# Kernel optimization log

Hardware: AMD Instinct MI355X
Metric: run time of the kernel (lower is better)

## Reference

```python
import jax, jax.numpy as jnp
import numpy as np
import math

N_BITS = 8
NUM_GROUPS = 32
NUM_HEADS = 8
EPS = 1e-5


def fake_quant(x):
    # UniformAffineQuantizer: dynamic per-tensor asymmetric 8-bit fake quant
    levels = 2 ** N_BITS - 1
    xmin = jnp.minimum(x.min(), 0.0)
    xmax = jnp.maximum(x.max(), 0.0)
    scale = jnp.maximum((xmax - xmin) / levels, 1e-8)
    zp = jnp.round(-xmin / scale)
    xq = jnp.clip(jnp.round(x / scale) + zp, 0, levels)
    return (xq - zp) * scale


def group_norm(x, w, b):
    # x: (B, C, T)
    B, C, T = x.shape
    xg = x.reshape(B, NUM_GROUPS, C // NUM_GROUPS, T)
    mean = xg.mean(axis=(2, 3), keepdims=True)
    var = xg.var(axis=(2, 3), keepdims=True)
    xg = (xg - mean) * jax.lax.rsqrt(var + EPS)
    return xg.reshape(B, C, T) * w[None, :, None] + b[None, :, None]


def setup_inputs() -> dict:
    key = jax.random.key(0)
    ks = jax.random.split(key, 7)
    C = 512
    x = jax.random.normal(ks[0], (8, C, 32, 32), dtype=jnp.float32)
    gn_w = jnp.ones((C,), jnp.float32)
    gn_b = jnp.zeros((C,), jnp.float32)
    qkv_w = jax.random.normal(ks[1], (3 * C, C), jnp.float32) * (1.0 / math.sqrt(C))
    qkv_b = jax.random.normal(ks[2], (3 * C,), jnp.float32) * 0.01
    proj_w = jax.random.normal(ks[3], (C, C), jnp.float32) * (1.0 / math.sqrt(C))
    proj_b = jax.random.normal(ks[4], (C,), jnp.float32) * 0.01
    return {"x": x, "gn_w": gn_w, "gn_b": gn_b, "qkv_w": qkv_w,
            "qkv_b": qkv_b, "proj_w": proj_w, "proj_b": proj_b}


def reference(x, gn_w, gn_b, qkv_w, qkv_b, proj_w, proj_b):
    b, c, *spatial = x.shape
    T = int(np.prod(spatial))
    xf = x.reshape(b, c, T)                       # (B, C, T)
    h = group_norm(xf, gn_w, gn_b)
    qkv = jnp.einsum('oc,bct->bot', qkv_w, h) + qkv_b[None, :, None]  # (B, 3C, T)
    qkv = qkv.reshape(b * NUM_HEADS, -1, T)       # (B*H, 3*ch, T)
    ch = qkv.shape[1] // 3
    q, k, v = jnp.split(qkv, 3, axis=1)
    q = fake_quant(q)
    k = fake_quant(k)
    v = fake_quant(v)
    scale = 1.0 / math.sqrt(math.sqrt(ch))
    w = jnp.einsum('bct,bcs->bts', q * scale, k * scale)
    w = jax.nn.softmax(w.astype(jnp.float32), axis=-1).astype(q.dtype)
    a = jnp.einsum('bts,bcs->bct', w, v)          # (B*H, ch, T)
    a = a.reshape(b, c, T)
    a = jnp.einsum('oc,bct->bot', proj_w, a) + proj_b[None, :, None]
    return (xf + a).reshape(b, c, *spatial)
```

## Files before the change

kernel.cpp:

```cpp
#include <hip/hip_runtime.h>

typedef __attribute__((ext_vector_type(8))) __bf16 bf16x8;
typedef __attribute__((ext_vector_type(4))) __bf16 bf16x4;
typedef __attribute__((ext_vector_type(4))) float  f32x4;


static constexpr size_t QKV_OFF = 0;
static constexpr size_t HT_OFF  = 50331648;
static constexpr size_t WQ_OFF  = HT_OFF + 8388608;
static constexpr size_t WP_OFF  = WQ_OFF + 1572864;
static constexpr size_t MM_OFF  = WP_OFF + 524288;
static constexpr size_t KI_OFF  = MM_OFF + 8192;
static constexpr size_t VI_OFF  = KI_OFF + 8388608;
static constexpr size_t QI_OFF  = VI_OFF + 8388608;
static constexpr size_t NEED_NEW = QI_OFF + 8388608;

__device__ __forceinline__ float dqi(float x, float inv_s, float zp) {
    float y = rintf(x * inv_s);
    return fminf(fmaxf(y, -zp), 255.0f - zp);
}
__device__ __forceinline__ f32x4 mfma16(bf16x8 a, bf16x8 b, f32x4 c) {
    return __builtin_amdgcn_mfma_f32_16x16x32_bf16(a, b, c, 0, 0, 0);
}
__device__ __forceinline__ float exp2i(float x) {
    float r;
    asm("v_exp_f32 %0, %1" : "=v"(r) : "v"(x));
    return r;
}
__device__ __forceinline__ void glds16(const __bf16* g, __bf16* l) {
    __builtin_amdgcn_global_load_lds((const __attribute__((address_space(1))) void*)g,
                                     (__attribute__((address_space(3))) void*)l, 16, 0, 0);
}
template <int N> __device__ __forceinline__ void waitv() {
    asm volatile("s_waitcnt vmcnt(%0)" :: "n"(N) : "memory");
}
__device__ __forceinline__ void bar_raw() {
    asm volatile("s_barrier" ::: "memory");
}

__device__ __forceinline__ void red_mm(const float* __restrict__ pmm, int id, int tid,
                                       float* sred, float& mn_out, float& mx_out) {
    float mn = pmm[id * 512 + tid * 2];
    float mx = pmm[id * 512 + tid * 2 + 1];
#pragma unroll
    for (int m = 1; m < 64; m <<= 1) {
        mn = fminf(mn, __shfl_xor(mn, m));
        mx = fmaxf(mx, __shfl_xor(mx, m));
    }
    if ((tid & 63) == 0) { sred[(tid >> 6) * 2] = mn; sred[(tid >> 6) * 2 + 1] = mx; }
    __syncthreads();
    mn = fminf(fminf(sred[0], sred[2]), fminf(sred[4], sred[6]));
    mx = fmaxf(fmaxf(sred[1], sred[3]), fmaxf(sred[5], sred[7]));
    __syncthreads();
    mn_out = fminf(mn, 0.0f);
    mx_out = fmaxf(mx, 0.0f);
}

__global__ __launch_bounds__(256) void gnprep(const float* __restrict__ x,
                                              const float* __restrict__ w,
                                              const float* __restrict__ bv,
                                              __bf16* __restrict__ hT,
                                              const float* __restrict__ qw,
                                              __bf16* __restrict__ wq,
                                              const float* __restrict__ pw,
                                              __bf16* __restrict__ wp) {
    int bid = blockIdx.x, tid = threadIdx.x;
    if (bid < 1024) {
        if (bid < 768) {
            int i = bid * 256 + tid;
            float4 v = ((const float4*)qw)[i];
            bf16x4 o = {(__bf16)v.x, (__bf16)v.y, (__bf16)v.z, (__bf16)v.w};
            ((bf16x4*)wq)[i] = o;
        } else {
            int i = (bid - 768) * 256 + tid;
            float4 v = ((const float4*)pw)[i];
            bf16x4 o = {(__bf16)v.x, (__bf16)v.y, (__bf16)v.z, (__bf16)v.w};
            ((bf16x4*)wp)[i] = o;
        }
        return;
    }
    int blk = bid - 1024;
    int b = blk >> 5, g = blk & 31;
    const float* xp = x + (size_t)(b * 512 + g * 16) * 1024;

    float4 v[16];
    float sum = 0.f, ss = 0.f;
#pragma unroll
    for (int i = 0; i < 16; ++i) {
        v[i] = *(const float4*)(xp + (size_t)i * 1024 + tid * 4);
        sum += v[i].x + v[i].y + v[i].z + v[i].w;
        ss  += v[i].x * v[i].x + v[i].y * v[i].y + v[i].z * v[i].z + v[i].w * v[i].w;
    }
#pragma unroll
    for (int m = 1; m < 64; m <<= 1) {
        sum += __shfl_xor(sum, m);
        ss  += __shfl_xor(ss, m);
    }
    __shared__ float s1[4], s2[4];
    int wid = tid >> 6;
    if ((tid & 63) == 0) { s1[wid] = sum; s2[wid] = ss; }
    __syncthreads();
    sum = s1[0] + s1[1] + s1[2] + s1[3];
    ss  = s2[0] + s2[1] + s2[2] + s2[3];
    float mean = sum * (1.0f / 16384.0f);
    float var  = ss * (1.0f / 16384.0f) - mean * mean;
    float rstd = rsqrtf(var + 1e-5f);

    float wc[16], bc[16];
#pragma unroll
    for (int c = 0; c < 16; ++c) { wc[c] = w[g * 16 + c] * rstd; bc[c] = bv[g * 16 + c]; }

#pragma unroll
    for (int j = 0; j < 4; ++j) {
        int t = tid * 4 + j;
        bf16x8 o0, o1;
#pragma unroll
        for (int c = 0; c < 8; ++c)
            o0[c] = (__bf16)(((&v[c].x)[j] - mean) * wc[c] + bc[c]);
#pragma unroll
        for (int c = 0; c < 8; ++c)
            o1[c] = (__bf16)(((&v[c + 8].x)[j] - mean) * wc[c + 8] + bc[c + 8]);
        __bf16* hp = hT + ((size_t)b * 1024 + t) * 512 + g * 16;
        *(bf16x8*)hp = o0;
        *(bf16x8*)(hp + 8) = o1;
    }
}

template <int MTILE, int MOT, bool MINMAX, bool RESID>
__global__ __launch_bounds__(256, 2) void mgemm5(const __bf16* __restrict__ A,
                                                 const __bf16* __restrict__ Bt,
                                                 const float* __restrict__ bias,
                                                 const float* __restrict__ resid,
                                                 float* __restrict__ out,
                                                 int M, float* __restrict__ pmm) {
    constexpr int NF  = (MTILE == 128) ? 4 : 2;
    constexpr int ASZ = MTILE * 64;
    constexpr int BSZ = 128 * 64;
    constexpr int LA  = MTILE / 32;
    constexpr int L   = LA + 4;
    constexpr int STG = 2 * (ASZ + BSZ) * 2;
    constexpr int CSB = 64 * 132 * 4;
    __shared__ __attribute__((aligned(16))) char smem_raw[(STG > CSB) ? STG : CSB];
    __bf16* sA0 = (__bf16*)smem_raw;
    __bf16* sA1 = sA0 + ASZ;
    __bf16* sB0 = sA1 + ASZ;
    __bf16* sB1 = sB0 + BSZ;
    __shared__ float smn[4], smx[4];

    int tid = threadIdx.x;
    int l = tid & 63, w = tid >> 6;
    int lo = l & 15, hi = l >> 4;

    int f = blockIdx.x;
    constexpr int NWG = MOT * 64;
    int wg = (f & 7) * (NWG / 8) + (f >> 3);
    int mo = wg % MOT, nb = wg / MOT;
    int nt = nb & 7, b = nb >> 3;

    const __bf16* Ap = A + (size_t)mo * MTILE * 512;
    const __bf16* Bp = Bt + ((size_t)b * 1024 + (size_t)nt * 128) * 512;
    int m0 = (MTILE == 128) ? (w >> 1) * 64 : 0;
    int n0 = (MTILE == 128) ? (w & 1) * 64 : w * 32;
    f32x4 acc[4][NF] = {};
    int scd = tid & 7;

    auto STAGE = [&](__bf16* dA, __bf16* dB, int k0) {
#pragma unroll
        for (int p = 0; p < LA; ++p) {
            int lin = p * 2048 + tid * 8;
            int row = lin >> 6;
            glds16(Ap + (size_t)row * 512 + k0 + ((scd ^ (row & 7)) << 3), dA + lin);
        }
#pragma unroll
        for (int p = 0; p < 4; ++p) {
            int lin = p * 2048 + tid * 8;
            int row = lin >> 6;
            glds16(Bp + (size_t)row * 512 + k0 + ((scd ^ (row & 7)) << 3), dB + lin);
        }
    };
    auto COMPUTE = [&](const __bf16* cA, const __bf16* cB) {
#pragma unroll
        for (int kk = 0; kk < 2; ++kk) {
            int rch = ((kk * 4 + hi) ^ (lo & 7)) << 3;
            bf16x8 af[4], bfr[NF];
#pragma unroll
            for (int i = 0; i < 4; ++i) af[i] = *(const bf16x8*)&cA[(m0 + 16 * i + lo) * 64 + rch];
#pragma unroll
            for (int j = 0; j < NF; ++j) bfr[j] = *(const bf16x8*)&cB[(n0 + 16 * j + lo) * 64 + rch];
#pragma unroll
            for (int i = 0; i < 4; ++i)
#pragma unroll
                for (int j = 0; j < NF; ++j) acc[i][j] = mfma16(af[i], bfr[j], acc[i][j]);
        }
    };

    STAGE(sA0, sB0, 0);
#pragma unroll
    for (int kp = 0; kp < 8; kp += 2) {
        if (kp + 1 < 8) { STAGE(sA1, sB1, (kp + 1) * 64); waitv<L>(); } else { waitv<0>(); }
        bar_raw();
        COMPUTE(sA0, sB0);
        bar_raw();
        if (kp + 2 < 8) { STAGE(sA0, sB0, (kp + 2) * 64); waitv<L>(); } else { waitv<0>(); }
        bar_raw();
        COMPUTE(sA1, sB1);
        bar_raw();
    }

    float* cs = (float*)smem_raw;
    float mn = 1e30f, mx = -1e30f;
    constexpr int NH = (MTILE == 128) ? 2 : 1;
#pragma unroll
    for (int h = 0; h < NH; ++h) {
        __syncthreads();
        if (MTILE == 64 || (w >> 1) == h) {
#pragma unroll
            for (int i = 0; i < 4; ++i)
#pragma unroll
                for (int r = 0; r < 4; ++r) {
                    int rl = 16 * i + hi * 4 + r;
                    float bi = bias[mo * MTILE + h * 64 + rl];
#pragma unroll
                    for (int j = 0; j < NF; ++j)
                        cs[rl * 132 + n0 + 16 * j + lo] = acc[i][j][r] + bi;
                }
        }
        __syncthreads();
#pragma unroll
        for (int it = 0; it < 8; ++it) {
            int lin = it * 256 + tid;
            int rr = lin >> 5, cc = (lin & 31) << 2;
            float4 v = *(const float4*)&cs[rr * 132 + cc];
            if (MINMAX) {
                mn = fminf(mn, fminf(fminf(v.x, v.y), fminf(v.z, v.w)));
                mx = fmaxf(mx, fmaxf(fmaxf(v.x, v.y), fmaxf(v.z, v.w)));
            }
            int grow = mo * MTILE + h * 64 + rr;
            size_t gaddr = ((size_t)b * M + grow) * 1024 + nt * 128 + cc;
            if (RESID) {
                float4 rv = *(const float4*)&resid[gaddr];
                v.x += rv.x; v.y += rv.y; v.z += rv.z; v.w += rv.w;
            }
            *(float4*)&out[gaddr] = v;
        }
    }

    if (MINMAX) {
#pragma unroll
        for (int msk = 1; msk < 64; msk <<= 1) {
            mn = fminf(mn, __shfl_xor(mn, msk));
            mx = fmaxf(mx, __shfl_xor(mx, msk));
        }
        if (l == 0) { smn[w] = mn; smx[w] = mx; }
        __syncthreads();
        if (tid == 0) {
            mn = fminf(fminf(smn[0], smn[1]), fminf(smn[2], smn[3]));
            mx = fmaxf(fmaxf(smx[0], smx[1]), fmaxf(smx[2], smx[3]));
            int id = mo >> 2;
            int slot = nb * 4 + (mo & 3);
            pmm[id * 512 + slot * 2]     = mn;
            pmm[id * 512 + slot * 2 + 1] = mx;
        }
    }
}

__global__ __launch_bounds__(256) void quant_qkv(const float* __restrict__ qkv,
                                                 const float* __restrict__ pmm,
                                                 __bf16* __restrict__ qi,
                                                 __bf16* __restrict__ ki,
                                                 __bf16* __restrict__ vi) {
    int bh = blockIdx.x, tt = blockIdx.y;
    int b = bh >> 3, hh = bh & 7;
    int t0 = tt * 64;
    const float* qg = qkv + (size_t)(b * 1536 + hh * 192) * 1024;
    const float* kg = qg + 65536;
    const float* vg = qg + 131072;
    int tid = threadIdx.x;

    __shared__ float sred[8];
    float mn0, mx0, mn1, mx1, mn2, mx2;
    red_mm(pmm, 0, tid, sred, mn0, mx0);
    red_mm(pmm, 1, tid, sred, mn1, mx1);
    red_mm(pmm, 2, tid, sred, mn2, mx2);
    float qsc = fmaxf((mx0 - mn0) * (1.f / 255.f), 1e-8f), qzp = rintf(-mn0 / qsc);
    float ksc = fmaxf((mx1 - mn1) * (1.f / 255.f), 1e-8f), kzp = rintf(-mn1 / ksc);
    float vsc = fmaxf((mx2 - mn2) * (1.f / 255.f), 1e-8f), vzp = rintf(-mn2 / vsc);
    float inv_q = 1.f / qsc, inv_k = 1.f / ksc, inv_v = 1.f / vsc;

    __shared__ __bf16 sT[64][68];
    int cr = tid >> 4, t4 = tid & 15;
    int s = tid >> 2, c0 = (tid & 3) * 16;

    __bf16* vd = vi + (size_t)bh * 65536;
#pragma unroll
    for (int r = 0; r < 4; ++r) {
        int c = 16 * r + cr;
        float4 v = *(const float4*)(vg + (size_t)c * 1024 + t0 + t4 * 4);
        bf16x4 o = {(__bf16)dqi(v.x, inv_v, vzp), (__bf16)dqi(v.y, inv_v, vzp),
                    (__bf16)dqi(v.z, inv_v, vzp), (__bf16)dqi(v.w, inv_v, vzp)};
        *(bf16x4*)(vd + (size_t)c * 1024 + t0 + t4 * 4) = o;
    }

#pragma unroll
    for (int r = 0; r < 4; ++r) {
        int c = 16 * r + cr;
        float4 v = *(const float4*)(kg + (size_t)c * 1024 + t0 + t4 * 4);
        sT[t4 * 4 + 0][c] = (__bf16)dqi(v.x, inv_k, kzp);
        sT[t4 * 4 + 1][c] = (__bf16)dqi(v.y, inv_k, kzp);
        sT[t4 * 4 + 2][c] = (__bf16)dqi(v.z, inv_k, kzp);
        sT[t4 * 4 + 3][c] = (__bf16)dqi(v.w, inv_k, kzp);
    }
    __syncthreads();
    {
        bf16x8 a0 = *(const bf16x8*)&sT[s][c0];
        bf16x8 a1 = *(const bf16x8*)&sT[s][c0 + 8];
        __bf16* kd = ki + ((size_t)bh * 1024 + t0 + s) * 64 + c0;
        *(bf16x8*)kd = a0;
        *(bf16x8*)(kd + 8) = a1;
    }
    __syncthreads();

#pragma unroll
    for (int r = 0; r < 4; ++r) {
        int c = 16 * r + cr;
        float4 v = *(const float4*)(qg + (size_t)c * 1024 + t0 + t4 * 4);
        sT[t4 * 4 + 0][c] = (__bf16)dqi(v.x, inv_q, qzp);
        sT[t4 * 4 + 1][c] = (__bf16)dqi(v.y, inv_q, qzp);
        sT[t4 * 4 + 2][c] = (__bf16)dqi(v.z, inv_q, qzp);
        sT[t4 * 4 + 3][c] = (__bf16)dqi(v.w, inv_q, qzp);
    }
    __syncthreads();
    {
        bf16x8 a0 = *(const bf16x8*)&sT[s][c0];
        bf16x8 a1 = *(const bf16x8*)&sT[s][c0 + 8];
        __bf16* qd = qi + ((size_t)bh * 1024 + t0 + s) * 64 + c0;
        *(bf16x8*)qd = a0;
        *(bf16x8*)(qd + 8) = a1;
    }
}

__global__ __launch_bounds__(256) void attn4(const __bf16* __restrict__ qi,
                                             const __bf16* __restrict__ ki,
                                             const __bf16* __restrict__ vi,
                                             const float* __restrict__ pmm,
                                             __bf16* __restrict__ aT) {
    int f = blockIdx.x;
    int bh = (f & 7) * 8 + ((f >> 3) & 7);
    int tt = f >> 6;
    int b = bh >> 3, hh = bh & 7;
    int t0 = tt * 64;
    const __bf16* kb = ki + (size_t)bh * 65536;
    const __bf16* vb = vi + (size_t)bh * 65536;
    int tid = threadIdx.x;

    __shared__ float sred[8];
    float mn0, mx0, mn1, mx1, mn2, mx2;
    red_mm(pmm, 0, tid, sred, mn0, mx0);
    red_mm(pmm, 1, tid, sred, mn1, mx1);
    red_mm(pmm, 2, tid, sred, mn2, mx2);
    float qsc = fmaxf((mx0 - mn0) * (1.f / 255.f), 1e-8f);
    float ksc = fmaxf((mx1 - mn1) * (1.f / 255.f), 1e-8f);
    float vsc = fmaxf((mx2 - mn2) * (1.f / 255.f), 1e-8f);
    float alpha2 = qsc * ksc * 0.125f * 1.4426950408889634f;
    float thr = 11.5415603f / alpha2;

    __shared__ __bf16 sh[64][72];
    __shared__ __bf16 kS[64 * 64];
    __shared__ __bf16 vS[64 * 64];
    int l = tid & 63, w = tid >> 6;
    int lo = l & 15, hi = l >> 4;

    const __bf16* qrow = qi + ((size_t)bh * 1024 + t0 + 16 * w + lo) * 64;
    bf16x8 qf0 = *(const bf16x8*)(qrow + hi * 8);
    bf16x8 qf1 = *(const bf16x8*)(qrow + 32 + hi * 8);

    int srow = tid >> 2, sc2 = (tid & 3) * 2;
    int swz0 = (sc2 ^ (srow & 7)) << 3;
    int swz1 = ((sc2 + 1) ^ (srow & 7)) << 3;
    const __bf16* kROW = kb + (size_t)srow * 64;
    const __bf16* vROW = vb + (size_t)srow * 1024;
    int lx = lo & 7;
    int rc0 = (hi ^ lx) << 3;
    int rc1 = ((4 + hi) ^ lx) << 3;

    bf16x8 kr0 = *(const bf16x8*)(kROW + sc2 * 8);
    bf16x8 kr1 = *(const bf16x8*)(kROW + sc2 * 8 + 8);
    bf16x8 vr0 = *(const bf16x8*)(vROW + sc2 * 8);
    bf16x8 vr1 = *(const bf16x8*)(vROW + sc2 * 8 + 8);

    f32x4 acc0 = {}, acc1 = {}, acc2 = {}, acc3 = {};
    float m_run = -1e30f, l_run = 0.f;

    for (int st = 0; st < 16; ++st) {
        __syncthreads();
        *(bf16x8*)(kS + srow * 64 + swz0) = kr0;
        *(bf16x8*)(kS + srow * 64 + swz1) = kr1;
        *(bf16x8*)(vS + srow * 64 + swz0) = vr0;
        *(bf16x8*)(vS + srow * 64 + swz1) = vr1;
        __syncthreads();
        if (st < 15) {
            kr0 = *(const bf16x8*)(kROW + (st + 1) * 4096 + sc2 * 8);
            kr1 = *(const bf16x8*)(kROW + (st + 1) * 4096 + sc2 * 8 + 8);
            vr0 = *(const bf16x8*)(vROW + (st + 1) * 64 + sc2 * 8);
            vr1 = *(const bf16x8*)(vROW + (st + 1) * 64 + sc2 * 8 + 8);
        }

        f32x4 sf[4] = {};
        __builtin_amdgcn_s_setprio(1);
#pragma unroll
        for (int sm = 0; sm < 4; ++sm)
            sf[sm] = mfma16(*(const bf16x8*)(kS + (16 * sm + lo) * 64 + rc0), qf0, sf[sm]);
#pragma unroll
        for (int sm = 0; sm < 4; ++sm)
            sf[sm] = mfma16(*(const bf16x8*)(kS + (16 * sm + lo) * 64 + rc1), qf1, sf[sm]);
        __builtin_amdgcn_s_setprio(0);

        float tm = -1e30f;
#pragma unroll
        for (int sm = 0; sm < 4; ++sm) {
            float a = fmaxf(sf[sm][0], sf[sm][1]);
            float c = fmaxf(sf[sm][2], sf[sm][3]);
            tm = fmaxf(tm, fmaxf(a, c));
        }
        tm = fmaxf(tm, __shfl_xor(tm, 16));
        tm = fmaxf(tm, __shfl_xor(tm, 32));
        if (!__all(tm <= m_run + thr)) {
            float mnew = fmaxf(m_run, tm);
            float fr = exp2i(alpha2 * (m_run - mnew));
            acc0 *= fr; acc1 *= fr; acc2 *= fr; acc3 *= fr;
            l_run *= fr;
            m_run = mnew;
        }
        float cc = -alpha2 * m_run;
        float ts = 0.f;
#pragma unroll
        for (int sm = 0; sm < 4; ++sm)
#pragma unroll
            for (int r = 0; r < 4; ++r) {
                float p = exp2i(fmaf(sf[sm][r], alpha2, cc));
                sf[sm][r] = p;
                ts += p;
            }
        ts += __shfl_xor(ts, 16);
        ts += __shfl_xor(ts, 32);
        l_run += ts;

#pragma unroll
        for (int sm = 0; sm < 4; ++sm) {
            bf16x4 pb = {(__bf16)sf[sm][0], (__bf16)sf[sm][1], (__bf16)sf[sm][2], (__bf16)sf[sm][3]};
            *(bf16x4*)&sh[16 * w + lo][16 * sm + hi * 4] = pb;
        }
        bf16x8 pf0 = *(const bf16x8*)&sh[16 * w + lo][hi * 8];
        bf16x8 pf1 = *(const bf16x8*)&sh[16 * w + lo][32 + hi * 8];

        __builtin_amdgcn_s_setprio(1);
        acc0 = mfma16(*(const bf16x8*)(vS + (lo) * 64 + rc0), pf0, acc0);
        acc1 = mfma16(*(const bf16x8*)(vS + (16 + lo) * 64 + rc0), pf0, acc1);
        acc2 = mfma16(*(const bf16x8*)(vS + (32 + lo) * 64 + rc0), pf0, acc2);
        acc3 = mfma16(*(const bf16x8*)(vS + (48 + lo) * 64 + rc0), pf0, acc3);
        acc0 = mfma16(*(const bf16x8*)(vS + (lo) * 64 + rc1), pf1, acc0);
        acc1 = mfma16(*(const bf16x8*)(vS + (16 + lo) * 64 + rc1), pf1, acc1);
        acc2 = mfma16(*(const bf16x8*)(vS + (32 + lo) * 64 + rc1), pf1, acc2);
        acc3 = mfma16(*(const bf16x8*)(vS + (48 + lo) * 64 + rc1), pf1, acc3);
        __builtin_amdgcn_s_setprio(0);
    }

    float rl = vsc / l_run;
    __syncthreads();
    {
        bf16x4 o0 = {(__bf16)(acc0[0] * rl), (__bf16)(acc0[1] * rl), (__bf16)(acc0[2] * rl), (__bf16)(acc0[3] * rl)};
        bf16x4 o1 = {(__bf16)(acc1[0] * rl), (__bf16)(acc1[1] * rl), (__bf16)(acc1[2] * rl), (__bf16)(acc1[3] * rl)};
        bf16x4 o2 = {(__bf16)(acc2[0] * rl), (__bf16)(acc2[1] * rl), (__bf16)(acc2[2] * rl), (__bf16)(acc2[3] * rl)};
        bf16x4 o3 = {(__bf16)(acc3[0] * rl), (__bf16)(acc3[1] * rl), (__bf16)(acc3[2] * rl), (__bf16)(acc3[3] * rl)};
        *(bf16x4*)&sh[16 * w + lo][0  + hi * 4] = o0;
        *(bf16x4*)&sh[16 * w + lo][16 + hi * 4] = o1;
        *(bf16x4*)&sh[16 * w + lo][32 + hi * 4] = o2;
        *(bf16x4*)&sh[16 * w + lo][48 + hi * 4] = o3;
    }
    __syncthreads();
    __bf16* ap = aT + ((size_t)b * 1024 + t0 + (tid >> 2)) * 512 + hh * 64;
    bf16x8 v0 = *(const bf16x8*)&sh[tid >> 2][(tid & 3) * 8];
    bf16x8 v1 = *(const bf16x8*)&sh[tid >> 2][32 + (tid & 3) * 8];
    *(bf16x8*)(ap + (tid & 3) * 8) = v0;
    *(bf16x8*)(ap + 32 + (tid & 3) * 8) = v1;
}

__global__ __launch_bounds__(256) void attn_mfma(const float* __restrict__ qkv,
                                                 const float* __restrict__ pmm,
                                                 __bf16* __restrict__ aT) {
    int f = blockIdx.x;
    int bh = (f & 7) * 8 + ((f >> 3) & 7);
    int tt = f >> 6;
    int b = bh >> 3, hh = bh & 7;
    int t0 = tt * 64;
    const float* qg = qkv + (size_t)(b * 1536 + hh * 192) * 1024;
    const float* kg = qg + (size_t)64 * 1024;
    const float* vg = qg + (size_t)128 * 1024;
    int tid = threadIdx.x;

    __shared__ float sred[8];
    float mn0, mx0, mn1, mx1, mn2, mx2;
    red_mm(pmm, 0, tid, sred, mn0, mx0);
    red_mm(pmm, 1, tid, sred, mn1, mx1);
    red_mm(pmm, 2, tid, sred, mn2, mx2);
    float qsc = fmaxf((mx0 - mn0) * (1.f / 255.f), 1e-8f), qzp = rintf(-mn0 / qsc);
    float ksc = fmaxf((mx1 - mn1) * (1.f / 255.f), 1e-8f), kzp = rintf(-mn1 / ksc);
    float vsc = fmaxf((mx2 - mn2) * (1.f / 255.f), 1e-8f), vzp = rintf(-mn2 / vsc);
    float inv_q = 1.f / qsc, inv_k = 1.f / ksc, inv_v = 1.f / vsc;
    float alpha = qsc * ksc * 0.125f;

    __shared__ __bf16 qT[64][72];
    __shared__ __bf16 kT[64][72];
    __shared__ __bf16 vL[64][72];
    __shared__ __bf16 pL[4][16][72];

    int l = tid & 63, w = tid >> 6;
    int lo = l & 15, hi = l >> 4;
    int c0 = (tid >> 4) * 4;
    int tl = tid & 15;

#pragma unroll
    for (int r = 0; r < 4; ++r) {
        int t = tl + 16 * r;
        float y0 = dqi(qg[(size_t)(c0 + 0) * 1024 + t0 + t], inv_q, qzp);
        float y1 = dqi(qg[(size_t)(c0 + 1) * 1024 + t0 + t], inv_q, qzp);
        float y2 = dqi(qg[(size_t)(c0 + 2) * 1024 + t0 + t], inv_q, qzp);
        float y3 = dqi(qg[(size_t)(c0 + 3) * 1024 + t0 + t], inv_q, qzp);
        bf16x4 o = {(__bf16)y0, (__bf16)y1, (__bf16)y2, (__bf16)y3};
        *(bf16x4*)&qT[t][c0] = o;
    }
    __syncthreads();
    bf16x8 qf0 = *(const bf16x8*)&qT[16 * w + lo][hi * 8];
    bf16x8 qf1 = *(const bf16x8*)&qT[16 * w + lo][32 + hi * 8];

    f32x4 acc0 = {}, acc1 = {}, acc2 = {}, acc3 = {};
    float m_run = -1e30f, l_run = 0.f;

    for (int st = 0; st < 16; ++st) {
        int s0 = st * 64;
        __syncthreads();
#pragma unroll
        for (int r = 0; r < 4; ++r) {
            int srow = tl + 16 * r;
            float y0 = dqi(kg[(size_t)(c0 + 0) * 1024 + s0 + srow], inv_k, kzp);
            float y1 = dqi(kg[(size_t)(c0 + 1) * 1024 + s0 + srow], inv_k, kzp);
            float y2 = dqi(kg[(size_t)(c0 + 2) * 1024 + s0 + srow], inv_k, kzp);
            float y3 = dqi(kg[(size_t)(c0 + 3) * 1024 + s0 + srow], inv_k, kzp);
            bf16x4 ok = {(__bf16)y0, (__bf16)y1, (__bf16)y2, (__bf16)y3};
            *(bf16x4*)&kT[srow][c0] = ok;
            int c = (tid >> 4) + 16 * r;
            float4 vv = *(const float4*)(vg + (size_t)c * 1024 + s0 + (tid & 15) * 4);
            bf16x4 ov = {(__bf16)dqi(vv.x, inv_v, vzp), (__bf16)dqi(vv.y, inv_v, vzp),
                         (__bf16)dqi(vv.z, inv_v, vzp), (__bf16)dqi(vv.w, inv_v, vzp)};
            *(bf16x4*)&vL[c][(tid & 15) * 4] = ov;
        }
        __syncthreads();

        f32x4 sf[4] = {};
#pragma unroll
        for (int sm = 0; sm < 4; ++sm)
            sf[sm] = mfma16(*(const bf16x8*)&kT[16 * sm + lo][hi * 8], qf0, sf[sm]);
#pragma unroll
        for (int sm = 0; sm < 4; ++sm)
            sf[sm] = mfma16(*(const bf16x8*)&kT[16 * sm + lo][32 + hi * 8], qf1, sf[sm]);

        float tm = -1e30f;
#pragma unroll
        for (int sm = 0; sm < 4; ++sm)
#pragma unroll
            for (int r = 0; r < 4; ++r) { sf[sm][r] *= alpha; tm = fmaxf(tm, sf[sm][r]); }
        tm = fmaxf(tm, __shfl_xor(tm, 16));
        tm = fmaxf(tm, __shfl_xor(tm, 32));
        float mnew = fmaxf(m_run, tm);
        float ts = 0.f;
#pragma unroll
        for (int sm = 0; sm < 4; ++sm)
#pragma unroll
            for (int r = 0; r < 4; ++r) {
                float p = __expf(sf[sm][r] - mnew);
                sf[sm][r] = p;
                ts += p;
            }
        ts += __shfl_xor(ts, 16);
        ts += __shfl_xor(ts, 32);
        float fr = __expf(m_run - mnew);
        l_run = l_run * fr + ts;
        m_run = mnew;
        acc0 *= fr; acc1 *= fr; acc2 *= fr; acc3 *= fr;

#pragma unroll
        for (int sm = 0; sm < 4; ++sm) {
            bf16x4 pb = {(__bf16)sf[sm][0], (__bf16)sf[sm][1], (__bf16)sf[sm][2], (__bf16)sf[sm][3]};
            *(bf16x4*)&pL[w][lo][16 * sm + hi * 4] = pb;
        }
        bf16x8 pf0 = *(const bf16x8*)&pL[w][lo][hi * 8];
        bf16x8 pf1 = *(const bf16x8*)&pL[w][lo][32 + hi * 8];
        acc0 = mfma16(*(const bf16x8*)&vL[lo][hi * 8], pf0, acc0);
        acc1 = mfma16(*(const bf16x8*)&vL[16 + lo][hi * 8], pf0, acc1);
        acc2 = mfma16(*(const bf16x8*)&vL[32 + lo][hi * 8], pf0, acc2);
        acc3 = mfma16(*(const bf16x8*)&vL[48 + lo][hi * 8], pf0, acc3);
        acc0 = mfma16(*(const bf16x8*)&vL[lo][32 + hi * 8], pf1, acc0);
        acc1 = mfma16(*(const bf16x8*)&vL[16 + lo][32 + hi * 8], pf1, acc1);
        acc2 = mfma16(*(const bf16x8*)&vL[32 + lo][32 + hi * 8], pf1, acc2);
        acc3 = mfma16(*(const bf16x8*)&vL[48 + lo][32 + hi * 8], pf1, acc3);
    }

    float rl = vsc / l_run;
    __syncthreads();
    {
        bf16x4 o0 = {(__bf16)(acc0[0] * rl), (__bf16)(acc0[1] * rl), (__bf16)(acc0[2] * rl), (__bf16)(acc0[3] * rl)};
        bf16x4 o1 = {(__bf16)(acc1[0] * rl), (__bf16)(acc1[1] * rl), (__bf16)(acc1[2] * rl), (__bf16)(acc1[3] * rl)};
        bf16x4 o2 = {(__bf16)(acc2[0] * rl), (__bf16)(acc2[1] * rl), (__bf16)(acc2[2] * rl), (__bf16)(acc2[3] * rl)};
        bf16x4 o3 = {(__bf16)(acc3[0] * rl), (__bf16)(acc3[1] * rl), (__bf16)(acc3[2] * rl), (__bf16)(acc3[3] * rl)};
        *(bf16x4*)&qT[16 * w + lo][0  + hi * 4] = o0;
        *(bf16x4*)&qT[16 * w + lo][16 + hi * 4] = o1;
        *(bf16x4*)&qT[16 * w + lo][32 + hi * 4] = o2;
        *(bf16x4*)&qT[16 * w + lo][48 + hi * 4] = o3;
    }
    __syncthreads();
    __bf16* ap = aT + ((size_t)b * 1024 + t0 + (tid >> 2)) * 512 + hh * 64;
    bf16x8 v0 = *(const bf16x8*)&qT[tid >> 2][(tid & 3) * 8];
    bf16x8 v1 = *(const bf16x8*)&qT[tid >> 2][32 + (tid & 3) * 8];
    *(bf16x8*)(ap + (tid & 3) * 8) = v0;
    *(bf16x8*)(ap + 32 + (tid & 3) * 8) = v1;
}

extern "C" void kernel_launch(void* const* d_in, const int* in_sizes, int n_in,
                              void* d_out, int out_size, void* d_ws, size_t ws_size,
                              hipStream_t stream) {
    const float* x      = (const float*)d_in[0];
    const float* gn_w   = (const float*)d_in[1];
    const float* gn_b   = (const float*)d_in[2];
    const float* qkv_w  = (const float*)d_in[3];
    const float* qkv_b  = (const float*)d_in[4];
    const float* proj_w = (const float*)d_in[5];
    const float* proj_b = (const float*)d_in[6];
    char* ws = (char*)d_ws;
    float*    qkv = (float*)(ws + QKV_OFF);
    __bf16*   hT  = (__bf16*)(ws + HT_OFF);
    __bf16*   wq  = (__bf16*)(ws + WQ_OFF);
    __bf16*   wp  = (__bf16*)(ws + WP_OFF);
    float*    pmm = (float*)(ws + MM_OFF);
    __bf16*   ki  = (__bf16*)(ws + KI_OFF);
    __bf16*   vi  = (__bf16*)(ws + VI_OFF);
    __bf16*   qi  = (__bf16*)(ws + QI_OFF);
    float* out = (float*)d_out;

    gnprep<<<1280, 256, 0, stream>>>(x, gn_w, gn_b, hT, qkv_w, wq, proj_w, wp);
    mgemm5<128, 12, true, false><<<768, 256, 0, stream>>>(wq, hT, qkv_b, nullptr, qkv, 1536, pmm);
    if (ws_size >= NEED_NEW) {
        quant_qkv<<<dim3(64, 16), 256, 0, stream>>>(qkv, pmm, qi, ki, vi);
        attn4<<<1024, 256, 0, stream>>>(qi, ki, vi, pmm, hT);
    } else {
        attn_mfma<<<1024, 256, 0, stream>>>(qkv, pmm, hT);
    }
    mgemm5<64, 8, false, true><<<512, 256, 0, stream>>>(wp, hT, proj_b, x, out, 512, nullptr);
}
```

Before: 104.8 us.

## Fuse Q quantization into attention with 128-query tiles and double-buffered K/V

The Q fake-quantization moves out of the separate quant kernel and into the attention kernel. Q is read directly from the fp32 QKV buffer and staged through LDS, so the intermediate bf16 Q buffer and its write-then-read round trip go away. The attention kernel now runs 512 threads over 128 query rows per block. This halves the number of blocks and lets each staged K/V tile serve twice as many queries. K/V tiles are double-buffered in LDS with one barrier per step instead of two, at the cost of more LDS per block and possibly lower occupancy.

```diff
diff --git a/kernel.cpp b/kernel.cpp
--- a/kernel.cpp
+++ b/kernel.cpp
@@ -12,8 +12,7 @@
 static constexpr size_t MM_OFF  = WP_OFF + 524288;
 static constexpr size_t KI_OFF  = MM_OFF + 8192;
 static constexpr size_t VI_OFF  = KI_OFF + 8388608;
-static constexpr size_t QI_OFF  = VI_OFF + 8388608;
-static constexpr size_t NEED_NEW = QI_OFF + 8388608;
+static constexpr size_t NEED_NEW = VI_OFF + 8388608;
 
 __device__ __forceinline__ float dqi(float x, float inv_s, float zp) {
     float y = rintf(x * inv_s);
@@ -51,6 +50,29 @@
     __syncthreads();
     mn = fminf(fminf(sred[0], sred[2]), fminf(sred[4], sred[6]));
     mx = fmaxf(fmaxf(sred[1], sred[3]), fmaxf(sred[5], sred[7]));
+    __syncthreads();
+    mn_out = fminf(mn, 0.0f);
+    mx_out = fmaxf(mx, 0.0f);
+}
+
+__device__ __forceinline__ void red_mm8(const float* __restrict__ pmm, int id, int tid,
+                                        float* sred, float& mn_out, float& mx_out) {
+    int slot = tid & 255;
+    float mn = pmm[id * 512 + slot * 2];
+    float mx = pmm[id * 512 + slot * 2 + 1];
+#pragma unroll
+    for (int m = 1; m < 64; m <<= 1) {
+        mn = fminf(mn, __shfl_xor(mn, m));
+        mx = fmaxf(mx, __shfl_xor(mx, m));
+    }
+    if ((tid & 63) == 0) { sred[(tid >> 6) * 2] = mn; sred[(tid >> 6) * 2 + 1] = mx; }
+    __syncthreads();
+    float a = fminf(fminf(sred[0], sred[2]), fminf(sred[4], sred[6]));
+    float b = fminf(fminf(sred[8], sred[10]), fminf(sred[12], sred[14]));
+    mn = fminf(a, b);
+    a = fmaxf(fmaxf(sred[1], sred[3]), fmaxf(sred[5], sred[7]));
+    b = fmaxf(fmaxf(sred[9], sred[11]), fmaxf(sred[13], sred[15]));
+    mx = fmaxf(a, b);
     __syncthreads();
     mn_out = fminf(mn, 0.0f);
     mx_out = fmaxf(mx, 0.0f);
@@ -264,28 +286,24 @@
     }
 }
 
-__global__ __launch_bounds__(256) void quant_qkv(const float* __restrict__ qkv,
-                                                 const float* __restrict__ pmm,
-                                                 __bf16* __restrict__ qi,
-                                                 __bf16* __restrict__ ki,
-                                                 __bf16* __restrict__ vi) {
+__global__ __launch_bounds__(256) void quant_kv(const float* __restrict__ qkv,
+                                                const float* __restrict__ pmm,
+                                                __bf16* __restrict__ ki,
+                                                __bf16* __restrict__ vi) {
     int bh = blockIdx.x, tt = blockIdx.y;
     int b = bh >> 3, hh = bh & 7;
     int t0 = tt * 64;
-    const float* qg = qkv + (size_t)(b * 1536 + hh * 192) * 1024;
-    const float* kg = qg + 65536;
-    const float* vg = qg + 131072;
+    const float* kg = qkv + ((size_t)(b * 1536 + hh * 192) + 64) * 1024;
+    const float* vg = kg + 65536;
     int tid = threadIdx.x;
 
     __shared__ float sred[8];
-    float mn0, mx0, mn1, mx1, mn2, mx2;
-    red_mm(pmm, 0, tid, sred, mn0, mx0);
+    float mn1, mx1, mn2, mx2;
     red_mm(pmm, 1, tid, sred, mn1, mx1);
     red_mm(pmm, 2, tid, sred, mn2, mx2);
-    float qsc = fmaxf((mx0 - mn0) * (1.f / 255.f), 1e-8f), qzp = rintf(-mn0 / qsc);
     float ksc = fmaxf((mx1 - mn1) * (1.f / 255.f), 1e-8f), kzp = rintf(-mn1 / ksc);
     float vsc = fmaxf((mx2 - mn2) * (1.f / 255.f), 1e-8f), vzp = rintf(-mn2 / vsc);
-    float inv_q = 1.f / qsc, inv_k = 1.f / ksc, inv_v = 1.f / vsc;
+    float inv_k = 1.f / ksc, inv_v = 1.f / vsc;
 
     __shared__ __bf16 sT[64][68];
     int cr = tid >> 4, t4 = tid & 15;
@@ -311,108 +329,97 @@
         sT[t4 * 4 + 3][c] = (__bf16)dqi(v.w, inv_k, kzp);
     }
     __syncthreads();
-    {
-        bf16x8 a0 = *(const bf16x8*)&sT[s][c0];
-        bf16x8 a1 = *(const bf16x8*)&sT[s][c0 + 8];
-        __bf16* kd = ki + ((size_t)bh * 1024 + t0 + s) * 64 + c0;
-        *(bf16x8*)kd = a0;
-        *(bf16x8*)(kd + 8) = a1;
-    }
-    __syncthreads();
-
-#pragma unroll
-    for (int r = 0; r < 4; ++r) {
-        int c = 16 * r + cr;
-        float4 v = *(const float4*)(qg + (size_t)c * 1024 + t0 + t4 * 4);
-        sT[t4 * 4 + 0][c] = (__bf16)dqi(v.x, inv_q, qzp);
-        sT[t4 * 4 + 1][c] = (__bf16)dqi(v.y, inv_q, qzp);
-        sT[t4 * 4 + 2][c] = (__bf16)dqi(v.z, inv_q, qzp);
-        sT[t4 * 4 + 3][c] = (__bf16)dqi(v.w, inv_q, qzp);
-    }
-    __syncthreads();
-    {
-        bf16x8 a0 = *(const bf16x8*)&sT[s][c0];
-        bf16x8 a1 = *(const bf16x8*)&sT[s][c0 + 8];
-        __bf16* qd = qi + ((size_t)bh * 1024 + t0 + s) * 64 + c0;
-        *(bf16x8*)qd = a0;
-        *(bf16x8*)(qd + 8) = a1;
-    }
-}
-
-__global__ __launch_bounds__(256) void attn4(const __bf16* __restrict__ qi,
-                                             const __bf16* __restrict__ ki,
-                                             const __bf16* __restrict__ vi,
-                                             const float* __restrict__ pmm,
-                                             __bf16* __restrict__ aT) {
+    bf16x8 a0 = *(const bf16x8*)&sT[s][c0];
+    bf16x8 a1 = *(const bf16x8*)&sT[s][c0 + 8];
+    __bf16* kd = ki + ((size_t)bh * 1024 + t0 + s) * 64 + c0;
+    *(bf16x8*)kd = a0;
+    *(bf16x8*)(kd + 8) = a1;
+}
+
+__global__ __launch_bounds__(512, 4) void attn5(const float* __restrict__ qkv,
+                                                const __bf16* __restrict__ ki,
+                                                const __bf16* __restrict__ vi,
+                                                const float* __restrict__ pmm,
+                                                __bf16* __restrict__ aT) {
     int f = blockIdx.x;
     int bh = (f & 7) * 8 + ((f >> 3) & 7);
     int tt = f >> 6;
     int b = bh >> 3, hh = bh & 7;
-    int t0 = tt * 64;
+    int t0 = tt * 128;
+    const float* qg = qkv + (size_t)(b * 1536 + hh * 192) * 1024;
     const __bf16* kb = ki + (size_t)bh * 65536;
     const __bf16* vb = vi + (size_t)bh * 65536;
     int tid = threadIdx.x;
 
-    __shared__ float sred[8];
+    __shared__ float sred[16];
     float mn0, mx0, mn1, mx1, mn2, mx2;
-    red_mm(pmm, 0, tid, sred, mn0, mx0);
-    red_mm(pmm, 1, tid, sred, mn1, mx1);
-    red_mm(pmm, 2, tid, sred, mn2, mx2);
-    float qsc = fmaxf((mx0 - mn0) * (1.f / 255.f), 1e-8f);
+    red_mm8(pmm, 0, tid, sred, mn0, mx0);
+    red_mm8(pmm, 1, tid, sred, mn1, mx1);
+    red_mm8(pmm, 2, tid, sred, mn2, mx2);
+    float qsc = fmaxf((mx0 - mn0) * (1.f / 255.f), 1e-8f), qzp = rintf(-mn0 / qsc);
     float ksc = fmaxf((mx1 - mn1) * (1.f / 255.f), 1e-8f);
     float vsc = fmaxf((mx2 - mn2) * (1.f / 255.f), 1e-8f);
+    float inv_q = 1.f / qsc;
     float alpha2 = qsc * ksc * 0.125f * 1.4426950408889634f;
     float thr = 11.5415603f / alpha2;
 
-    __shared__ __bf16 sh[64][72];
-    __shared__ __bf16 kS[64 * 64];
-    __shared__ __bf16 vS[64 * 64];
+    __shared__ __bf16 sh[128][72];
+    __shared__ __bf16 kS[2][4096];
+    __shared__ __bf16 vS[2][4096];
     int l = tid & 63, w = tid >> 6;
     int lo = l & 15, hi = l >> 4;
 
-    const __bf16* qrow = qi + ((size_t)bh * 1024 + t0 + 16 * w + lo) * 64;
-    bf16x8 qf0 = *(const bf16x8*)(qrow + hi * 8);
-    bf16x8 qf1 = *(const bf16x8*)(qrow + 32 + hi * 8);
-
-    int srow = tid >> 2, sc2 = (tid & 3) * 2;
-    int swz0 = (sc2 ^ (srow & 7)) << 3;
-    int swz1 = ((sc2 + 1) ^ (srow & 7)) << 3;
+    int srow = tid >> 3, sc = tid & 7;
+    int swz = (sc ^ (srow & 7)) << 3;
     const __bf16* kROW = kb + (size_t)srow * 64;
     const __bf16* vROW = vb + (size_t)srow * 1024;
     int lx = lo & 7;
     int rc0 = (hi ^ lx) << 3;
     int rc1 = ((4 + hi) ^ lx) << 3;
 
-    bf16x8 kr0 = *(const bf16x8*)(kROW + sc2 * 8);
-    bf16x8 kr1 = *(const bf16x8*)(kROW + sc2 * 8 + 8);
-    bf16x8 vr0 = *(const bf16x8*)(vROW + sc2 * 8);
-    bf16x8 vr1 = *(const bf16x8*)(vROW + sc2 * 8 + 8);
+    bf16x8 kr = *(const bf16x8*)(kROW + sc * 8);
+    bf16x8 vr = *(const bf16x8*)(vROW + sc * 8);
+
+    {
+        int c0 = (tid >> 5) * 4;
+        int tl = tid & 31;
+#pragma unroll
+        for (int r = 0; r < 4; ++r) {
+            int t = tl + 32 * r;
+            float y0 = dqi(qg[(size_t)(c0 + 0) * 1024 + t0 + t], inv_q, qzp);
+            float y1 = dqi(qg[(size_t)(c0 + 1) * 1024 + t0 + t], inv_q, qzp);
+            float y2 = dqi(qg[(size_t)(c0 + 2) * 1024 + t0 + t], inv_q, qzp);
+            float y3 = dqi(qg[(size_t)(c0 + 3) * 1024 + t0 + t], inv_q, qzp);
+            bf16x4 o = {(__bf16)y0, (__bf16)y1, (__bf16)y2, (__bf16)y3};
+            *(bf16x4*)&sh[t][c0] = o;
+        }
+    }
+    __syncthreads();
+    bf16x8 qf0 = *(const bf16x8*)&sh[16 * w + lo][hi * 8];
+    bf16x8 qf1 = *(const bf16x8*)&sh[16 * w + lo][32 + hi * 8];
+    *(bf16x8*)(kS[0] + srow * 64 + swz) = kr;
+    *(bf16x8*)(vS[0] + srow * 64 + swz) = vr;
+    __syncthreads();
 
     f32x4 acc0 = {}, acc1 = {}, acc2 = {}, acc3 = {};
     float m_run = -1e30f, l_run = 0.f;
 
     for (int st = 0; st < 16; ++st) {
-        __syncthreads();
-        *(bf16x8*)(kS + srow * 64 + swz0) = kr0;
-        *(bf16x8*)(kS + srow * 64 + swz1) = kr1;
-        *(bf16x8*)(vS + srow * 64 + swz0) = vr0;
-        *(bf16x8*)(vS + srow * 64 + swz1) = vr1;
-        __syncthreads();
+        const __bf16* kc = kS[st & 1];
+        const __bf16* vc = vS[st & 1];
         if (st < 15) {
-            kr0 = *(const bf16x8*)(kROW + (st + 1) * 4096 + sc2 * 8);
-            kr1 = *(const bf16x8*)(kROW + (st + 1) * 4096 + sc2 * 8 + 8);
-            vr0 = *(const bf16x8*)(vROW + (st + 1) * 64 + sc2 * 8);
-            vr1 = *(const bf16x8*)(vROW + (st + 1) * 64 + sc2 * 8 + 8);
+            kr = *(const bf16x8*)(kROW + (st + 1) * 4096 + sc * 8);
+            vr = *(const bf16x8*)(vROW + (st + 1) * 64 + sc * 8);
         }
 
         f32x4 sf[4] = {};
         __builtin_amdgcn_s_setprio(1);
 #pragma unroll
         for (int sm = 0; sm < 4; ++sm)
-            sf[sm] = mfma16(*(const bf16x8*)(kS + (16 * sm + lo) * 64 + rc0), qf0, sf[sm]);
+            sf[sm] = mfma16(*(const bf16x8*)(kc + (16 * sm + lo) * 64 + rc0), qf0, sf[sm]);
 #pragma unroll
         for (int sm = 0; sm < 4; ++sm)
-            sf[sm] = mfma16(*(const bf16x8*)(kS + (16 * sm + lo) * 64 + rc1), qf1, sf[sm]);
+            sf[sm] = mfma16(*(const bf16x8*)(kc + (16 * sm + lo) * 64 + rc1), qf1, sf[sm]);
         __builtin_amdgcn_s_setprio(0);
 
         float tm = -1e30f;
@@ -454,19 +461,24 @@
         bf16x8 pf1 = *(const bf16x8*)&sh[16 * w + lo][32 + hi * 8];
 
         __builtin_amdgcn_s_setprio(1);
-        acc0 = mfma16(*(const bf16x8*)(vS + (lo) * 64 + rc0), pf0, acc0);
-        acc1 = mfma16(*(const bf16x8*)(vS + (16 + lo) * 64 + rc0), pf0, acc1);
-        acc2 = mfma16(*(const bf16x8*)(vS + (32 + lo) * 64 + rc0), pf0, acc2);
-        acc3 = mfma16(*(const bf16x8*)(vS + (48 + lo) * 64 + rc0), pf0, acc3);
-        acc0 = mfma16(*(const bf16x8*)(vS + (lo) * 64 + rc1), pf1, acc0);
-        acc1 = mfma16(*(const bf16x8*)(vS + (16 + lo) * 64 + rc1), pf1, acc1);
-        acc2 = mfma16(*(const bf16x8*)(vS + (32 + lo) * 64 + rc1), pf1, acc2);
-        acc3 = mfma16(*(const bf16x8*)(vS + (48 + lo) * 64 + rc1), pf1, acc3);
+        acc0 = mfma16(*(const bf16x8*)(vc + (lo) * 64 + rc0), pf0, acc0);
+        acc1 = mfma16(*(const bf16x8*)(vc + (16 + lo) * 64 + rc0), pf0, acc1);
+        acc2 = mfma16(*(const bf16x8*)(vc + (32 + lo) * 64 + rc0), pf0, acc2);
+        acc3 = mfma16(*(const bf16x8*)(vc + (48 + lo) * 64 + rc0), pf0, acc3);
+        acc0 = mfma16(*(const bf16x8*)(vc + (lo) * 64 + rc1), pf1, acc0);
+        acc1 = mfma16(*(const bf16x8*)(vc + (16 + lo) * 64 + rc1), pf1, acc1);
+        acc2 = mfma16(*(const bf16x8*)(vc + (32 + lo) * 64 + rc1), pf1, acc2);
+        acc3 = mfma16(*(const bf16x8*)(vc + (48 + lo) * 64 + rc1), pf1, acc3);
         __builtin_amdgcn_s_setprio(0);
+
+        if (st < 15) {
+            *(bf16x8*)(kS[(st + 1) & 1] + srow * 64 + swz) = kr;
+            *(bf16x8*)(vS[(st + 1) & 1] + srow * 64 + swz) = vr;
+        }
+        __syncthreads();
     }
 
     float rl = vsc / l_run;
-    __syncthreads();
     {
         bf16x4 o0 = {(__bf16)(acc0[0] * rl), (__bf16)(acc0[1] * rl), (__bf16)(acc0[2] * rl), (__bf16)(acc0[3] * rl)};
         bf16x4 o1 = {(__bf16)(acc1[0] * rl), (__bf16)(acc1[1] * rl), (__bf16)(acc1[2] * rl), (__bf16)(acc1[3] * rl)};
@@ -643,14 +655,13 @@
     float*    pmm = (float*)(ws + MM_OFF);
     __bf16*   ki  = (__bf16*)(ws + KI_OFF);
     __bf16*   vi  = (__bf16*)(ws + VI_OFF);
-    __bf16*   qi  = (__bf16*)(ws + QI_OFF);
     float* out = (float*)d_out;
 
     gnprep<<<1280, 256, 0, stream>>>(x, gn_w, gn_b, hT, qkv_w, wq, proj_w, wp);
     mgemm5<128, 12, true, false><<<768, 256, 0, stream>>>(wq, hT, qkv_b, nullptr, qkv, 1536, pmm);
     if (ws_size >= NEED_NEW) {
-        quant_qkv<<<dim3(64, 16), 256, 0, stream>>>(qkv, pmm, qi, ki, vi);
-        attn4<<<1024, 256, 0, stream>>>(qi, ki, vi, pmm, hT);
+        quant_kv<<<dim3(64, 16), 256, 0, stream>>>(qkv, pmm, ki, vi);
+        attn5<<<512, 512, 0, stream>>>(qkv, ki, vi, pmm, hT);
     } else {
         attn_mfma<<<1024, 256, 0, stream>>>(qkv, pmm, hT);
     }
```

Result: faster. 92.64 us (-11.6%).
